# Kernel tuning notes

Measured on AMD Instinct MI355X. Metric: run time of the kernel, lower is better.

## Reference

```python
import jax, jax.numpy as jnp
import numpy as np

L = 5          # num_layer
D = 128        # emb_dim
F = 16         # raw node/edge feature dim
N = 50000      # nodes
E = 800000     # edges
BN_EPS = 1e-5


def _bn(z, g, b):
    # BatchNorm1d forward with batch statistics (training-mode math)
    m = z.mean(axis=0)
    v = z.var(axis=0)
    return (z - m) * jax.lax.rsqrt(v + BN_EPS) * g + b


def setup_inputs() -> dict:
    key = jax.random.key(0)
    ks = jax.random.split(key, 8)
    s = lambda *sh: 0.05  # weight scale
    return {
        "x": jax.random.normal(ks[0], (N, F), jnp.float32),
        "edge_index": jax.random.randint(ks[1], (2, E), 0, N, jnp.int32),
        "edge_attr": jax.random.normal(ks[2], (E, F), jnp.float32),
        "W_node": jax.random.normal(ks[3], (F, D), jnp.float32) * 0.05,
        "b_node": jnp.zeros((D,), jnp.float32),
        "We": jax.random.normal(ks[4], (L, F, D), jnp.float32) * 0.05,
        "be": jnp.zeros((L, D), jnp.float32),
        "eps_gin": jnp.zeros((L,), jnp.float32),
        "W1": jax.random.normal(ks[5], (L, D, 2 * D), jnp.float32) * 0.05,
        "b1": jnp.zeros((L, 2 * D), jnp.float32),
        "g1": jnp.ones((L, 2 * D), jnp.float32),
        "beta1": jnp.zeros((L, 2 * D), jnp.float32),
        "W2": jax.random.normal(ks[6], (L, 2 * D, D), jnp.float32) * 0.05,
        "b2": jnp.zeros((L, D), jnp.float32),
        "g_bn": jnp.ones((L, D), jnp.float32),
        "beta_bn": jnp.zeros((L, D), jnp.float32),
    }


def reference(x, edge_index, edge_attr, W_node, b_node, We, be, eps_gin,
              W1, b1, g1, beta1, W2, b2, g_bn, beta_bn):
    src, dst = edge_index[0], edge_index[1]
    n = x.shape[0]
    h = x @ W_node + b_node                       # node encoder: [N, D]
    for l in range(L):
        e = edge_attr @ We[l] + be[l]             # edge encoder: [E, D]
        msg = jax.nn.relu(h[src] + e)             # gather + message
        agg = jax.ops.segment_sum(msg, dst, num_segments=n)  # scatter-add
        z = (1.0 + eps_gin[l]) * h + agg
        z = _bn(z @ W1[l] + b1[l], g1[l], beta1[l])  # GIN MLP hidden
        z = jax.nn.relu(z)
        z = z @ W2[l] + b2[l]                     # GIN MLP out: [N, D]
        z = _bn(z, g_bn[l], beta_bn[l])           # per-layer BatchNorm
        if l < L - 1:
            z = jax.nn.relu(z)                    # dropout is identity (p=0)
        h = z + h                                 # residual
    return h                                      # JK = 'last'
```

## Files before the change

kernel.cpp:

```cpp
#include <hip/hip_runtime.h>
#include <hip/hip_bf16.h>

#define NN 50000
#define EE 800000
#define DD 128
#define FF 16
#define LL 5
#define NB 782
#define NPART (NB * 4)

typedef __attribute__((ext_vector_type(8))) short bf16x8;
typedef __attribute__((ext_vector_type(4))) float f32x4;

__device__ __forceinline__ unsigned short f2bf(float f) {
    union { float f; unsigned int u; } v; v.f = f;
    unsigned int u = v.u;
    unsigned int r = (u + 0x7fffu + ((u >> 16) & 1u)) >> 16;
    return (unsigned short)r;
}
__device__ __forceinline__ float bf2f(unsigned short s) {
    union { unsigned int u; float f; } v; v.u = ((unsigned int)s) << 16;
    return v.f;
}
#define BFLO(u) __uint_as_float((unsigned int)(u) << 16)
#define BFHI(u) __uint_as_float((unsigned int)(u) & 0xffff0000u)

__global__ void k_node_enc(const float* __restrict__ x, const float* __restrict__ Wn,
                           const float* __restrict__ bn, float* __restrict__ h,
                           unsigned short* __restrict__ h_bf)
{
    const int t = blockIdx.x * 256 + threadIdx.x;
    const int i = t >> 7, d = t & 127;
    const float4* x4 = (const float4*)(x + (size_t)i * 16);
    float4 a0 = x4[0], a1 = x4[1], a2 = x4[2], a3 = x4[3];
    float acc = bn[d];
    acc += a0.x*Wn[0*128+d] + a0.y*Wn[1*128+d] + a0.z*Wn[2*128+d] + a0.w*Wn[3*128+d];
    acc += a1.x*Wn[4*128+d] + a1.y*Wn[5*128+d] + a1.z*Wn[6*128+d] + a1.w*Wn[7*128+d];
    acc += a2.x*Wn[8*128+d] + a2.y*Wn[9*128+d] + a2.z*Wn[10*128+d] + a2.w*Wn[11*128+d];
    acc += a3.x*Wn[12*128+d] + a3.y*Wn[13*128+d] + a3.z*Wn[14*128+d] + a3.w*Wn[15*128+d];
    h[t] = acc;
    h_bf[t] = f2bf(acc);
}

__global__ void k_count(const int* __restrict__ ei, int* __restrict__ counts)
{
    const int e = blockIdx.x * 256 + threadIdx.x;
    atomicAdd(&counts[ei[EE + e]], 1);
}

__global__ __launch_bounds__(1024) void k_scan(int* __restrict__ counts, int* __restrict__ row_ptr)
{
    __shared__ int wsum[16];
    __shared__ int carry;
    const int tid = threadIdx.x, lane = tid & 63, w = tid >> 6;
    if (tid == 0) carry = 0;
    __syncthreads();
    for (int base = 0; base < NN; base += 1024) {
        const int i = base + tid;
        const int v = (i < NN) ? counts[i] : 0;
        int x = v;
        #pragma unroll
        for (int off = 1; off < 64; off <<= 1) {
            const int t = __shfl_up(x, off);
            if (lane >= off) x += t;
        }
        if (lane == 63) wsum[w] = x;
        __syncthreads();
        int woff = 0, total = 0;
        #pragma unroll
        for (int j = 0; j < 16; ++j) { const int s = wsum[j]; total += s; if (j < w) woff += s; }
        const int ex = carry + woff + x - v;
        if (i < NN) { row_ptr[i] = ex; counts[i] = ex; }
        __syncthreads();
        if (tid == 0) carry += total;
        __syncthreads();
    }
    if (tid == 0) row_ptr[NN] = carry;
}

__global__ void k_fill(const int* __restrict__ ei, const float* __restrict__ ea,
                       int* __restrict__ cursor, int* __restrict__ src_perm,
                       unsigned short* __restrict__ ea_bf)
{
    const int e = blockIdx.x * 256 + threadIdx.x;
    const int dst = ei[EE + e];
    const int p = atomicAdd(&cursor[dst], 1);
    src_perm[p] = ei[e];
    const float4* s4 = (const float4*)(ea + (size_t)e * 16);
    const float4 a0 = s4[0], a1 = s4[1], a2 = s4[2], a3 = s4[3];
    union { bf16x8 v; unsigned short u[8]; } o0, o1;
    o0.u[0]=f2bf(a0.x); o0.u[1]=f2bf(a0.y); o0.u[2]=f2bf(a0.z); o0.u[3]=f2bf(a0.w);
    o0.u[4]=f2bf(a1.x); o0.u[5]=f2bf(a1.y); o0.u[6]=f2bf(a1.z); o0.u[7]=f2bf(a1.w);
    o1.u[0]=f2bf(a2.x); o1.u[1]=f2bf(a2.y); o1.u[2]=f2bf(a2.z); o1.u[3]=f2bf(a2.w);
    o1.u[4]=f2bf(a3.x); o1.u[5]=f2bf(a3.y); o1.u[6]=f2bf(a3.z); o1.u[7]=f2bf(a3.w);
    bf16x8* dp = (bf16x8*)(ea_bf + (size_t)p * 16);
    dp[0] = o0.v; dp[1] = o1.v;
}

__global__ void k_pack(const float* __restrict__ W1, const float* __restrict__ W2,
                       unsigned short* __restrict__ Wp1, unsigned short* __restrict__ Wp2)
{
    int t = blockIdx.x * 256 + threadIdx.x;
    const int total = LL * 32768;
    if (t < total) {
        const int l = t >> 15, r = t & 32767;
        const int j = r & 7, lane = (r >> 3) & 63, kt = (r >> 9) & 3, nt = r >> 11;
        const int k = kt * 32 + (lane >> 4) * 8 + j;
        const int n = nt * 16 + (lane & 15);
        Wp1[t] = f2bf(W1[(size_t)l * 32768 + k * 256 + n]);
    } else {
        t -= total;
        const int l = t >> 15, r = t & 32767;
        const int j = r & 7, lane = (r >> 3) & 63, kt = (r >> 9) & 7, nt = r >> 12;
        const int k = kt * 32 + (lane >> 4) * 8 + j;
        const int n = nt * 16 + (lane & 15);
        Wp2[t] = f2bf(W2[(size_t)l * 32768 + k * 128 + n]);
    }
}

__global__ __launch_bounds__(256) void k_agg(
    const unsigned short* __restrict__ h_bf, const unsigned short* __restrict__ ea_bf,
    const float* __restrict__ We_l, const float* __restrict__ be_l,
    const float* __restrict__ eps_gin, const int l,
    const int* __restrict__ row_ptr, const int* __restrict__ src_perm,
    unsigned short* __restrict__ z_bf)
{
    const int wv = threadIdx.x >> 6;
    const int v  = blockIdx.x * 4 + wv;
    const int lane = threadIdx.x & 63;
    const int c2 = lane * 2;
    float2 w[16];
    #pragma unroll
    for (int f = 0; f < 16; ++f) w[f] = *(const float2*)(We_l + f * 128 + c2);
    const float2 bed = *(const float2*)(be_l + c2);
    const float epsv = 1.0f + eps_gin[l];
    const int kbeg = __builtin_amdgcn_readfirstlane(row_ptr[v]);
    const int kend = __builtin_amdgcn_readfirstlane(row_ptr[v + 1]);
    float2 acc0 = {0.f,0.f}, acc1 = {0.f,0.f}, acc2 = {0.f,0.f}, acc3 = {0.f,0.f};

#define EDGE_DOT(EA, EB, HQ, OUT) do {                                      \
        float ex_ = bed.x, ey_ = bed.y, a_;                                 \
        a_ = BFLO(EA.x); ex_ += a_*w[0].x;  ey_ += a_*w[0].y;               \
        a_ = BFHI(EA.x); ex_ += a_*w[1].x;  ey_ += a_*w[1].y;               \
        a_ = BFLO(EA.y); ex_ += a_*w[2].x;  ey_ += a_*w[2].y;               \
        a_ = BFHI(EA.y); ex_ += a_*w[3].x;  ey_ += a_*w[3].y;               \
        a_ = BFLO(EA.z); ex_ += a_*w[4].x;  ey_ += a_*w[4].y;               \
        a_ = BFHI(EA.z); ex_ += a_*w[5].x;  ey_ += a_*w[5].y;               \
        a_ = BFLO(EA.w); ex_ += a_*w[6].x;  ey_ += a_*w[6].y;               \
        a_ = BFHI(EA.w); ex_ += a_*w[7].x;  ey_ += a_*w[7].y;               \
        a_ = BFLO(EB.x); ex_ += a_*w[8].x;  ey_ += a_*w[8].y;               \
        a_ = BFHI(EB.x); ex_ += a_*w[9].x;  ey_ += a_*w[9].y;               \
        a_ = BFLO(EB.y); ex_ += a_*w[10].x; ey_ += a_*w[10].y;              \
        a_ = BFHI(EB.y); ex_ += a_*w[11].x; ey_ += a_*w[11].y;              \
        a_ = BFLO(EB.z); ex_ += a_*w[12].x; ey_ += a_*w[12].y;              \
        a_ = BFHI(EB.z); ex_ += a_*w[13].x; ey_ += a_*w[13].y;              \
        a_ = BFLO(EB.w); ex_ += a_*w[14].x; ey_ += a_*w[14].y;              \
        a_ = BFHI(EB.w); ex_ += a_*w[15].x; ey_ += a_*w[15].y;              \
        const float mx_ = BFLO(HQ) + ex_, my_ = BFHI(HQ) + ey_;             \
        OUT.x += mx_ > 0.f ? mx_ : 0.f;                                     \
        OUT.y += my_ > 0.f ? my_ : 0.f;                                     \
    } while (0)

    uint4 ce0, ce1, ce2, ce3, ce4, ce5, ce6, ce7;
    unsigned int ch0, ch1, ch2, ch3;
    int vs0, vs1, vs2, vs3;

    int k = kbeg;
    if (k < kend) {
        const int a0 = __builtin_amdgcn_readfirstlane(src_perm[k]);
        const int a1 = __builtin_amdgcn_readfirstlane(src_perm[k + 1]);
        const int a2 = __builtin_amdgcn_readfirstlane(src_perm[k + 2]);
        const int a3 = __builtin_amdgcn_readfirstlane(src_perm[k + 3]);
        ch0 = *(const unsigned int*)(h_bf + (size_t)a0 * 128 + c2);
        ch1 = *(const unsigned int*)(h_bf + (size_t)a1 * 128 + c2);
        ch2 = *(const unsigned int*)(h_bf + (size_t)a2 * 128 + c2);
        ch3 = *(const unsigned int*)(h_bf + (size_t)a3 * 128 + c2);
        const uint4* ep = (const uint4*)(ea_bf + (size_t)k * 16);
        ce0 = ep[0]; ce1 = ep[1]; ce2 = ep[2]; ce3 = ep[3];
        ce4 = ep[4]; ce5 = ep[5]; ce6 = ep[6]; ce7 = ep[7];
        vs0 = src_perm[k + 4]; vs1 = src_perm[k + 5];
        vs2 = src_perm[k + 6]; vs3 = src_perm[k + 7];
    }
    for (; k < kend; k += 4) {
        const int fs0 = src_perm[k + 8],  fs1 = src_perm[k + 9];
        const int fs2 = src_perm[k + 10], fs3 = src_perm[k + 11];
        const int b0 = __builtin_amdgcn_readfirstlane(vs0);
        const int b1 = __builtin_amdgcn_readfirstlane(vs1);
        const int b2 = __builtin_amdgcn_readfirstlane(vs2);
        const int b3 = __builtin_amdgcn_readfirstlane(vs3);
        const unsigned int nh0 = *(const unsigned int*)(h_bf + (size_t)b0 * 128 + c2);
        const unsigned int nh1 = *(const unsigned int*)(h_bf + (size_t)b1 * 128 + c2);
        const unsigned int nh2 = *(const unsigned int*)(h_bf + (size_t)b2 * 128 + c2);
        const unsigned int nh3 = *(const unsigned int*)(h_bf + (size_t)b3 * 128 + c2);
        const uint4* np_ = (const uint4*)(ea_bf + (size_t)(k + 4) * 16);
        const uint4 ne0 = np_[0], ne1 = np_[1], ne2 = np_[2], ne3 = np_[3];
        const uint4 ne4 = np_[4], ne5 = np_[5], ne6 = np_[6], ne7 = np_[7];
        __builtin_amdgcn_sched_barrier(0);
        EDGE_DOT(ce0, ce1, ch0, acc0);
        if (k + 1 < kend) EDGE_DOT(ce2, ce3, ch1, acc1);
        if (k + 2 < kend) EDGE_DOT(ce4, ce5, ch2, acc2);
        if (k + 3 < kend) EDGE_DOT(ce6, ce7, ch3, acc3);
        ce0=ne0; ce1=ne1; ce2=ne2; ce3=ne3; ce4=ne4; ce5=ne5; ce6=ne6; ce7=ne7;
        ch0=nh0; ch1=nh1; ch2=nh2; ch3=nh3;
        vs0=fs0; vs1=fs1; vs2=fs2; vs3=fs3;
    }
#undef EDGE_DOT
    const unsigned int hv = *(const unsigned int*)(h_bf + (size_t)v * 128 + c2);
    const float zx = epsv * BFLO(hv) + ((acc0.x + acc1.x) + (acc2.x + acc3.x));
    const float zy = epsv * BFHI(hv) + ((acc0.y + acc1.y) + (acc2.y + acc3.y));
    const unsigned int zp = (unsigned int)f2bf(zx) | ((unsigned int)f2bf(zy) << 16);
    *(unsigned int*)(z_bf + (size_t)v * 128 + c2) = zp;
}

__global__ __launch_bounds__(256) void k_gemmB(
    const unsigned short* __restrict__ z_bf,
    const unsigned short* __restrict__ Wp,
    unsigned short* __restrict__ t_bf,
    float* __restrict__ ps, float* __restrict__ pq)
{
    __shared__ __align__(16) unsigned short zs[64 * 136];
    const int tid = threadIdx.x;
    const int r0 = blockIdx.x * 64;
    {
        const int rb = tid >> 4, c0 = (tid & 15) * 8;
        const bf16x8 zero = {0,0,0,0,0,0,0,0};
        #pragma unroll
        for (int r = 0; r < 4; ++r) {
            const int row = r * 16 + rb, g = r0 + row;
            *(bf16x8*)(&zs[row * 136 + c0]) =
                (g < NN) ? *(const bf16x8*)(z_bf + (size_t)g * 128 + c0) : zero;
        }
    }
    __syncthreads();
    const int w = tid >> 6, l6 = tid & 63, m = l6 & 15, quad = l6 >> 4;
    const f32x4 z4 = {0.f, 0.f, 0.f, 0.f};
    f32x4 acc[16] = {z4,z4,z4,z4,z4,z4,z4,z4,z4,z4,z4,z4,z4,z4,z4,z4};
    const bf16x8* Wv = (const bf16x8*)Wp;
    #pragma unroll
    for (int kt = 0; kt < 4; ++kt) {
        const bf16x8 a = *(const bf16x8*)(&zs[(w * 16 + m) * 136 + kt * 32 + quad * 8]);
        #pragma unroll
        for (int ct = 0; ct < 16; ++ct) {
            const bf16x8 b = Wv[(ct * 4 + kt) * 64 + l6];
            acc[ct] = __builtin_amdgcn_mfma_f32_16x16x32_bf16(a, b, acc[ct], 0, 0, 0);
        }
    }
    const int rowb = r0 + w * 16 + quad * 4;
    #pragma unroll
    for (int ct = 0; ct < 16; ++ct) {
        const int col = ct * 16 + m;
        float ssum = 0.f, ssq = 0.f;
        #pragma unroll
        for (int r = 0; r < 4; ++r) {
            const float val = acc[ct][r];
            if (rowb + r < NN) t_bf[(size_t)(rowb + r) * 256 + col] = f2bf(val);
            ssum += val; ssq += val * val;
        }
        ssum += __shfl_xor(ssum, 16); ssum += __shfl_xor(ssum, 32);
        ssq  += __shfl_xor(ssq , 16); ssq  += __shfl_xor(ssq , 32);
        if (quad == 0) {
            ps[(size_t)col * NPART + blockIdx.x * 4 + w] = ssum;
            pq[(size_t)col * NPART + blockIdx.x * 4 + w] = ssq;
        }
    }
}

__global__ void k_bnstat(const float* __restrict__ ps, const float* __restrict__ pq,
                         const float* __restrict__ g, const float* __restrict__ beta,
                         float* __restrict__ sc, float* __restrict__ sh)
{
    const int c = blockIdx.x;
    const int tid = threadIdx.x;
    const float* pr = ps + (size_t)c * NPART;
    const float* qr = pq + (size_t)c * NPART;
    float s = 0.f, q = 0.f;
    for (int i = tid; i < NPART; i += 256) { s += pr[i]; q += qr[i]; }
    #pragma unroll
    for (int off = 1; off < 64; off <<= 1) { s += __shfl_xor(s, off); q += __shfl_xor(q, off); }
    __shared__ float ls[4], lq[4];
    const int wv = tid >> 6;
    if ((tid & 63) == 0) { ls[wv] = s; lq[wv] = q; }
    __syncthreads();
    if (tid == 0) {
        const float S = ls[0] + ls[1] + ls[2] + ls[3];
        const float Q = lq[0] + lq[1] + lq[2] + lq[3];
        const float mean = S * (1.0f / NN);
        const float var  = Q * (1.0f / NN) - mean * mean;
        const float rs = rsqrtf(var + 1e-5f);
        const float scale = g[c] * rs;
        sc[c] = scale;
        sh[c] = beta[c] - mean * scale;
    }
}

__global__ __launch_bounds__(256) void k_gemmD(
    const unsigned short* __restrict__ t_bf,
    const float* __restrict__ sc1, const float* __restrict__ sh1,
    const unsigned short* __restrict__ Wp,
    unsigned short* __restrict__ vb,
    float* __restrict__ ps, float* __restrict__ pq)
{
    __shared__ __align__(16) unsigned short us[64 * 264];
    const int tid = threadIdx.x;
    const int r0 = blockIdx.x * 64;
    {
        const int rb = tid >> 5, c0 = (tid & 31) * 8;
        const float4 s0 = *(const float4*)(sc1 + c0), s1 = *(const float4*)(sc1 + c0 + 4);
        const float4 b0 = *(const float4*)(sh1 + c0), b1 = *(const float4*)(sh1 + c0 + 4);
        const bf16x8 zero = {0,0,0,0,0,0,0,0};
        #pragma unroll
        for (int rr = 0; rr < 8; ++rr) {
            const int row = rr * 8 + rb, g = r0 + row;
            union { bf16x8 v; unsigned short u[8]; } in, o;
            if (g < NN) {
                in.v = *(const bf16x8*)(t_bf + (size_t)g * 256 + c0);
                float xv;
                xv = bf2f(in.u[0])*s0.x + b0.x; o.u[0] = f2bf(xv > 0.f ? xv : 0.f);
                xv = bf2f(in.u[1])*s0.y + b0.y; o.u[1] = f2bf(xv > 0.f ? xv : 0.f);
                xv = bf2f(in.u[2])*s0.z + b0.z; o.u[2] = f2bf(xv > 0.f ? xv : 0.f);
                xv = bf2f(in.u[3])*s0.w + b0.w; o.u[3] = f2bf(xv > 0.f ? xv : 0.f);
                xv = bf2f(in.u[4])*s1.x + b1.x; o.u[4] = f2bf(xv > 0.f ? xv : 0.f);
                xv = bf2f(in.u[5])*s1.y + b1.y; o.u[5] = f2bf(xv > 0.f ? xv : 0.f);
                xv = bf2f(in.u[6])*s1.z + b1.z; o.u[6] = f2bf(xv > 0.f ? xv : 0.f);
                xv = bf2f(in.u[7])*s1.w + b1.w; o.u[7] = f2bf(xv > 0.f ? xv : 0.f);
            } else {
                o.v = zero;
            }
            *(bf16x8*)(&us[row * 264 + c0]) = o.v;
        }
    }
    __syncthreads();
    const int w = tid >> 6, l6 = tid & 63, m = l6 & 15, quad = l6 >> 4;
    const f32x4 z4 = {0.f, 0.f, 0.f, 0.f};
    f32x4 acc[8] = {z4,z4,z4,z4,z4,z4,z4,z4};
    const bf16x8* Wv = (const bf16x8*)Wp;
    #pragma unroll
    for (int kt = 0; kt < 8; ++kt) {
        const bf16x8 a = *(const bf16x8*)(&us[(w * 16 + m) * 264 + kt * 32 + quad * 8]);
        #pragma unroll
        for (int ct = 0; ct < 8; ++ct) {
            const bf16x8 b = Wv[(ct * 8 + kt) * 64 + l6];
            acc[ct] = __builtin_amdgcn_mfma_f32_16x16x32_bf16(a, b, acc[ct], 0, 0, 0);
        }
    }
    const int rowb = r0 + w * 16 + quad * 4;
    #pragma unroll
    for (int ct = 0; ct < 8; ++ct) {
        const int col = ct * 16 + m;
        float ssum = 0.f, ssq = 0.f;
        #pragma unroll
        for (int r = 0; r < 4; ++r) {
            const float val = acc[ct][r];
            if (rowb + r < NN) vb[(size_t)(rowb + r) * 128 + col] = f2bf(val);
            ssum += val; ssq += val * val;
        }
        ssum += __shfl_xor(ssum, 16); ssum += __shfl_xor(ssum, 32);
        ssq  += __shfl_xor(ssq , 16); ssq  += __shfl_xor(ssq , 32);
        if (quad == 0) {
            ps[(size_t)col * NPART + blockIdx.x * 4 + w] = ssum;
            pq[(size_t)col * NPART + blockIdx.x * 4 + w] = ssq;
        }
    }
}

__global__ void k_fin(const unsigned short* __restrict__ vb,
                      const float* __restrict__ sc2, const float* __restrict__ sh2,
                      float* __restrict__ h, unsigned short* __restrict__ h_bf,
                      const int do_relu)
{
    const int t = blockIdx.x * 256 + threadIdx.x;
    const int base = t * 8;
    const int c = base & 127;
    union { bf16x8 v; unsigned short u[8]; } in, ob;
    in.v = *(const bf16x8*)(vb + base);
    const float4 s0 = *(const float4*)(sc2 + c), s1 = *(const float4*)(sc2 + c + 4);
    const float4 b0 = *(const float4*)(sh2 + c), b1 = *(const float4*)(sh2 + c + 4);
    float4 h0 = *(const float4*)(h + base), h1 = *(const float4*)(h + base + 4);
    float z;
    z = bf2f(in.u[0])*s0.x + b0.x; if (do_relu) z = z > 0.f ? z : 0.f; h0.x += z;
    z = bf2f(in.u[1])*s0.y + b0.y; if (do_relu) z = z > 0.f ? z : 0.f; h0.y += z;
    z = bf2f(in.u[2])*s0.z + b0.z; if (do_relu) z = z > 0.f ? z : 0.f; h0.z += z;
    z = bf2f(in.u[3])*s0.w + b0.w; if (do_relu) z = z > 0.f ? z : 0.f; h0.w += z;
    z = bf2f(in.u[4])*s1.x + b1.x; if (do_relu) z = z > 0.f ? z : 0.f; h1.x += z;
    z = bf2f(in.u[5])*s1.y + b1.y; if (do_relu) z = z > 0.f ? z : 0.f; h1.y += z;
    z = bf2f(in.u[6])*s1.z + b1.z; if (do_relu) z = z > 0.f ? z : 0.f; h1.z += z;
    z = bf2f(in.u[7])*s1.w + b1.w; if (do_relu) z = z > 0.f ? z : 0.f; h1.w += z;
    *(float4*)(h + base) = h0;
    *(float4*)(h + base + 4) = h1;
    ob.u[0]=f2bf(h0.x); ob.u[1]=f2bf(h0.y); ob.u[2]=f2bf(h0.z); ob.u[3]=f2bf(h0.w);
    ob.u[4]=f2bf(h1.x); ob.u[5]=f2bf(h1.y); ob.u[6]=f2bf(h1.z); ob.u[7]=f2bf(h1.w);
    *(bf16x8*)(h_bf + base) = ob.v;
}

extern "C" void kernel_launch(void* const* d_in, const int* in_sizes, int n_in,
                              void* d_out, int out_size, void* d_ws, size_t ws_size,
                              hipStream_t stream)
{
    const float* x       = (const float*)d_in[0];
    const int*   ei      = (const int*)  d_in[1];
    const float* ea      = (const float*)d_in[2];
    const float* W_node  = (const float*)d_in[3];
    const float* b_node  = (const float*)d_in[4];
    const float* We      = (const float*)d_in[5];
    const float* be      = (const float*)d_in[6];
    const float* eps_gin = (const float*)d_in[7];
    const float* W1      = (const float*)d_in[8];
    const float* g1      = (const float*)d_in[10];
    const float* beta1   = (const float*)d_in[11];
    const float* W2      = (const float*)d_in[12];
    const float* g_bn    = (const float*)d_in[14];
    const float* beta_bn = (const float*)d_in[15];

    float* h = (float*)d_out;

    char* W = (char*)d_ws;
    int*   counts   = (int*)  (W + 0);
    int*   row_ptr  = (int*)  (W + 200000);
    float* sc1      = (float*)(W + 400064);
    float* sh1      = (float*)(W + 401088);
    float* sc2      = (float*)(W + 402112);
    float* sh2      = (float*)(W + 402624);
    float* ps1      = (float*)(W + 403136);
    float* pq1      = (float*)(W + 3606208);
    float* ps2      = (float*)(W + 6809280);
    float* pq2      = (float*)(W + 8410816);
    int*   src_perm = (int*)  (W + 10012352);
    unsigned short* ea_bf = (unsigned short*)(W + 13212416);
    unsigned short* Wp1   = (unsigned short*)(W + 38812928);
    unsigned short* Wp2   = (unsigned short*)(W + 39140608);
    unsigned short* z_bf  = (unsigned short*)(W + 39468288);
    unsigned short* t_bf  = (unsigned short*)(W + 52268288);
    unsigned short* h_bf  = (unsigned short*)(W + 77868288);
    unsigned short* vb    = z_bf;

    (void)hipMemsetAsync(counts, 0, 200000, stream);
    (void)hipMemsetAsync(src_perm + EE, 0, 64, stream);

    k_node_enc<<<dim3(NN * DD / 256), dim3(256), 0, stream>>>(x, W_node, b_node, h, h_bf);
    k_count<<<dim3(EE / 256), dim3(256), 0, stream>>>(ei, counts);
    k_scan<<<dim3(1), dim3(1024), 0, stream>>>(counts, row_ptr);
    k_fill<<<dim3(EE / 256), dim3(256), 0, stream>>>(ei, ea, counts, src_perm, ea_bf);
    k_pack<<<dim3(2 * LL * 32768 / 256), dim3(256), 0, stream>>>(W1, W2, Wp1, Wp2);

    for (int l = 0; l < LL; ++l) {
        k_agg<<<dim3(NN / 4), dim3(256), 0, stream>>>(
            h_bf, ea_bf, We + (size_t)l * FF * DD, be + (size_t)l * DD,
            eps_gin, l, row_ptr, src_perm, z_bf);
        k_gemmB<<<dim3(NB), dim3(256), 0, stream>>>(
            z_bf, Wp1 + (size_t)l * 32768, t_bf, ps1, pq1);
        k_bnstat<<<dim3(256), dim3(256), 0, stream>>>(
            ps1, pq1, g1 + (size_t)l * 256, beta1 + (size_t)l * 256, sc1, sh1);
        k_gemmD<<<dim3(NB), dim3(256), 0, stream>>>(
            t_bf, sc1, sh1, Wp2 + (size_t)l * 32768, vb, ps2, pq2);
        k_bnstat<<<dim3(128), dim3(256), 0, stream>>>(
            ps2, pq2, g_bn + (size_t)l * 128, beta_bn + (size_t)l * 128, sc2, sh2);
        k_fin<<<dim3(NN * DD / 8 / 256), dim3(256), 0, stream>>>(
            vb, sc2, sh2, h, h_bf, (l < LL - 1) ? 1 : 0);
    }
}
```

Baseline: 1.051 ms.

## Fuse BN statistics via atomics and hold weight tiles in registers for GEMMs

```diff
diff --git a/kernel.cpp b/kernel.cpp
--- a/kernel.cpp
+++ b/kernel.cpp
@@ -7,7 +7,6 @@
 #define FF 16
 #define LL 5
 #define NB 782
-#define NPART (NB * 4)
 
 typedef __attribute__((ext_vector_type(8))) short bf16x8;
 typedef __attribute__((ext_vector_type(4))) float f32x4;
@@ -216,97 +215,95 @@
     const unsigned short* __restrict__ z_bf,
     const unsigned short* __restrict__ Wp,
     unsigned short* __restrict__ t_bf,
-    float* __restrict__ ps, float* __restrict__ pq)
-{
-    __shared__ __align__(16) unsigned short zs[64 * 136];
+    float* __restrict__ ps1, float* __restrict__ pq1)
+{
     const int tid = threadIdx.x;
+    const int w = tid >> 6, l6 = tid & 63, m = l6 & 15, quad = l6 >> 4;
     const int r0 = blockIdx.x * 64;
+    const bf16x8* Wv = (const bf16x8*)Wp;
+    bf16x8 b[4][4];
+    #pragma unroll
+    for (int ct = 0; ct < 4; ++ct)
+        #pragma unroll
+        for (int kt = 0; kt < 4; ++kt)
+            b[ct][kt] = Wv[((w * 4 + ct) * 4 + kt) * 64 + l6];
+
+    const bf16x8 zero8 = {0,0,0,0,0,0,0,0};
+    const f32x4 z4 = {0.f, 0.f, 0.f, 0.f};
+    float rs_[4] = {0.f,0.f,0.f,0.f}, rq_[4] = {0.f,0.f,0.f,0.f};
+
+    bf16x8 a[4], an[4];
     {
-        const int rb = tid >> 4, c0 = (tid & 15) * 8;
-        const bf16x8 zero = {0,0,0,0,0,0,0,0};
-        #pragma unroll
-        for (int r = 0; r < 4; ++r) {
-            const int row = r * 16 + rb, g = r0 + row;
-            *(bf16x8*)(&zs[row * 136 + c0]) =
-                (g < NN) ? *(const bf16x8*)(z_bf + (size_t)g * 128 + c0) : zero;
-        }
-    }
-    __syncthreads();
-    const int w = tid >> 6, l6 = tid & 63, m = l6 & 15, quad = l6 >> 4;
-    const f32x4 z4 = {0.f, 0.f, 0.f, 0.f};
-    f32x4 acc[16] = {z4,z4,z4,z4,z4,z4,z4,z4,z4,z4,z4,z4,z4,z4,z4,z4};
-    const bf16x8* Wv = (const bf16x8*)Wp;
-    #pragma unroll
-    for (int kt = 0; kt < 4; ++kt) {
-        const bf16x8 a = *(const bf16x8*)(&zs[(w * 16 + m) * 136 + kt * 32 + quad * 8]);
-        #pragma unroll
-        for (int ct = 0; ct < 16; ++ct) {
-            const bf16x8 b = Wv[(ct * 4 + kt) * 64 + l6];
-            acc[ct] = __builtin_amdgcn_mfma_f32_16x16x32_bf16(a, b, acc[ct], 0, 0, 0);
-        }
-    }
-    const int rowb = r0 + w * 16 + quad * 4;
-    #pragma unroll
-    for (int ct = 0; ct < 16; ++ct) {
-        const int col = ct * 16 + m;
-        float ssum = 0.f, ssq = 0.f;
-        #pragma unroll
-        for (int r = 0; r < 4; ++r) {
-            const float val = acc[ct][r];
-            if (rowb + r < NN) t_bf[(size_t)(rowb + r) * 256 + col] = f2bf(val);
-            ssum += val; ssq += val * val;
-        }
-        ssum += __shfl_xor(ssum, 16); ssum += __shfl_xor(ssum, 32);
-        ssq  += __shfl_xor(ssq , 16); ssq  += __shfl_xor(ssq , 32);
+        const int row = r0 + m;
+        #pragma unroll
+        for (int kt = 0; kt < 4; ++kt)
+            a[kt] = (row < NN) ? *(const bf16x8*)(z_bf + (size_t)row * 128 + kt * 32 + quad * 8) : zero8;
+    }
+    #pragma unroll
+    for (int rt = 0; rt < 4; ++rt) {
+        if (rt < 3) {
+            const int row = r0 + (rt + 1) * 16 + m;
+            #pragma unroll
+            for (int kt = 0; kt < 4; ++kt)
+                an[kt] = (row < NN) ? *(const bf16x8*)(z_bf + (size_t)row * 128 + kt * 32 + quad * 8) : zero8;
+        }
+        f32x4 acc[4] = {z4, z4, z4, z4};
+        #pragma unroll
+        for (int kt = 0; kt < 4; ++kt)
+            #pragma unroll
+            for (int ct = 0; ct < 4; ++ct)
+                acc[ct] = __builtin_amdgcn_mfma_f32_16x16x32_bf16(a[kt], b[ct][kt], acc[ct], 0, 0, 0);
+        const int rowb = r0 + rt * 16 + quad * 4;
+        #pragma unroll
+        for (int ct = 0; ct < 4; ++ct) {
+            const int col = w * 64 + ct * 16 + m;
+            #pragma unroll
+            for (int r = 0; r < 4; ++r) {
+                const float val = acc[ct][r];
+                if (rowb + r < NN) t_bf[(size_t)(rowb + r) * 256 + col] = f2bf(val);
+                rs_[ct] += val; rq_[ct] += val * val;
+            }
+        }
+        #pragma unroll
+        for (int kt = 0; kt < 4; ++kt) a[kt] = an[kt];
+    }
+    #pragma unroll
+    for (int ct = 0; ct < 4; ++ct) {
+        float ss = rs_[ct], sq = rq_[ct];
+        ss += __shfl_xor(ss, 16); ss += __shfl_xor(ss, 32);
+        sq += __shfl_xor(sq, 16); sq += __shfl_xor(sq, 32);
         if (quad == 0) {
-            ps[(size_t)col * NPART + blockIdx.x * 4 + w] = ssum;
-            pq[(size_t)col * NPART + blockIdx.x * 4 + w] = ssq;
-        }
-    }
-}
-
-__global__ void k_bnstat(const float* __restrict__ ps, const float* __restrict__ pq,
-                         const float* __restrict__ g, const float* __restrict__ beta,
-                         float* __restrict__ sc, float* __restrict__ sh)
-{
-    const int c = blockIdx.x;
-    const int tid = threadIdx.x;
-    const float* pr = ps + (size_t)c * NPART;
-    const float* qr = pq + (size_t)c * NPART;
-    float s = 0.f, q = 0.f;
-    for (int i = tid; i < NPART; i += 256) { s += pr[i]; q += qr[i]; }
-    #pragma unroll
-    for (int off = 1; off < 64; off <<= 1) { s += __shfl_xor(s, off); q += __shfl_xor(q, off); }
-    __shared__ float ls[4], lq[4];
-    const int wv = tid >> 6;
-    if ((tid & 63) == 0) { ls[wv] = s; lq[wv] = q; }
-    __syncthreads();
-    if (tid == 0) {
-        const float S = ls[0] + ls[1] + ls[2] + ls[3];
-        const float Q = lq[0] + lq[1] + lq[2] + lq[3];
-        const float mean = S * (1.0f / NN);
-        const float var  = Q * (1.0f / NN) - mean * mean;
-        const float rs = rsqrtf(var + 1e-5f);
-        const float scale = g[c] * rs;
-        sc[c] = scale;
-        sh[c] = beta[c] - mean * scale;
+            const int col = w * 64 + ct * 16 + m;
+            atomicAdd(&ps1[col], ss);
+            atomicAdd(&pq1[col], sq);
+        }
     }
 }
 
 __global__ __launch_bounds__(256) void k_gemmD(
     const unsigned short* __restrict__ t_bf,
-    const float* __restrict__ sc1, const float* __restrict__ sh1,
+    const float* __restrict__ ps1, const float* __restrict__ pq1,
+    const float* __restrict__ g1, const float* __restrict__ be1,
     const unsigned short* __restrict__ Wp,
     unsigned short* __restrict__ vb,
-    float* __restrict__ ps, float* __restrict__ pq)
+    float* __restrict__ ps2, float* __restrict__ pq2)
 {
     __shared__ __align__(16) unsigned short us[64 * 264];
+    __shared__ __align__(16) float scf[256], shf[256];
     const int tid = threadIdx.x;
+    {
+        const float mean = ps1[tid] * (1.0f / NN);
+        const float var  = pq1[tid] * (1.0f / NN) - mean * mean;
+        const float sc = g1[tid] * rsqrtf(var + 1e-5f);
+        scf[tid] = sc;
+        shf[tid] = be1[tid] - mean * sc;
+    }
+    __syncthreads();
     const int r0 = blockIdx.x * 64;
     {
         const int rb = tid >> 5, c0 = (tid & 31) * 8;
-        const float4 s0 = *(const float4*)(sc1 + c0), s1 = *(const float4*)(sc1 + c0 + 4);
-        const float4 b0 = *(const float4*)(sh1 + c0), b1 = *(const float4*)(sh1 + c0 + 4);
+        const float4 s0 = *(const float4*)(scf + c0), s1 = *(const float4*)(scf + c0 + 4);
+        const float4 b0 = *(const float4*)(shf + c0), b1 = *(const float4*)(shf + c0 + 4);
         const bf16x8 zero = {0,0,0,0,0,0,0,0};
         #pragma unroll
         for (int rr = 0; rr < 8; ++rr) {
@@ -331,50 +328,76 @@
     }
     __syncthreads();
     const int w = tid >> 6, l6 = tid & 63, m = l6 & 15, quad = l6 >> 4;
+    const bf16x8* Wv = (const bf16x8*)Wp;
+    bf16x8 b[2][8];
+    #pragma unroll
+    for (int ct = 0; ct < 2; ++ct)
+        #pragma unroll
+        for (int kt = 0; kt < 8; ++kt)
+            b[ct][kt] = Wv[((w * 2 + ct) * 8 + kt) * 64 + l6];
+
     const f32x4 z4 = {0.f, 0.f, 0.f, 0.f};
-    f32x4 acc[8] = {z4,z4,z4,z4,z4,z4,z4,z4};
-    const bf16x8* Wv = (const bf16x8*)Wp;
-    #pragma unroll
-    for (int kt = 0; kt < 8; ++kt) {
-        const bf16x8 a = *(const bf16x8*)(&us[(w * 16 + m) * 264 + kt * 32 + quad * 8]);
-        #pragma unroll
-        for (int ct = 0; ct < 8; ++ct) {
-            const bf16x8 b = Wv[(ct * 8 + kt) * 64 + l6];
-            acc[ct] = __builtin_amdgcn_mfma_f32_16x16x32_bf16(a, b, acc[ct], 0, 0, 0);
-        }
-    }
-    const int rowb = r0 + w * 16 + quad * 4;
-    #pragma unroll
-    for (int ct = 0; ct < 8; ++ct) {
-        const int col = ct * 16 + m;
-        float ssum = 0.f, ssq = 0.f;
-        #pragma unroll
-        for (int r = 0; r < 4; ++r) {
-            const float val = acc[ct][r];
-            if (rowb + r < NN) vb[(size_t)(rowb + r) * 128 + col] = f2bf(val);
-            ssum += val; ssq += val * val;
-        }
-        ssum += __shfl_xor(ssum, 16); ssum += __shfl_xor(ssum, 32);
-        ssq  += __shfl_xor(ssq , 16); ssq  += __shfl_xor(ssq , 32);
+    float rs_[2] = {0.f,0.f}, rq_[2] = {0.f,0.f};
+    #pragma unroll
+    for (int rt = 0; rt < 4; ++rt) {
+        bf16x8 a[8];
+        #pragma unroll
+        for (int kt = 0; kt < 8; ++kt)
+            a[kt] = *(const bf16x8*)(&us[(rt * 16 + m) * 264 + kt * 32 + quad * 8]);
+        f32x4 acc[2] = {z4, z4};
+        #pragma unroll
+        for (int kt = 0; kt < 8; ++kt)
+            #pragma unroll
+            for (int ct = 0; ct < 2; ++ct)
+                acc[ct] = __builtin_amdgcn_mfma_f32_16x16x32_bf16(a[kt], b[ct][kt], acc[ct], 0, 0, 0);
+        const int rowb = r0 + rt * 16 + quad * 4;
+        #pragma unroll
+        for (int ct = 0; ct < 2; ++ct) {
+            const int col = w * 32 + ct * 16 + m;
+            #pragma unroll
+            for (int r = 0; r < 4; ++r) {
+                const float val = acc[ct][r];
+                if (rowb + r < NN) vb[(size_t)(rowb + r) * 128 + col] = f2bf(val);
+                rs_[ct] += val; rq_[ct] += val * val;
+            }
+        }
+    }
+    #pragma unroll
+    for (int ct = 0; ct < 2; ++ct) {
+        float ss = rs_[ct], sq = rq_[ct];
+        ss += __shfl_xor(ss, 16); ss += __shfl_xor(ss, 32);
+        sq += __shfl_xor(sq, 16); sq += __shfl_xor(sq, 32);
         if (quad == 0) {
-            ps[(size_t)col * NPART + blockIdx.x * 4 + w] = ssum;
-            pq[(size_t)col * NPART + blockIdx.x * 4 + w] = ssq;
+            const int col = w * 32 + ct * 16 + m;
+            atomicAdd(&ps2[col], ss);
+            atomicAdd(&pq2[col], sq);
         }
     }
 }
 
 __global__ void k_fin(const unsigned short* __restrict__ vb,
-                      const float* __restrict__ sc2, const float* __restrict__ sh2,
+                      const float* __restrict__ ps2, const float* __restrict__ pq2,
+                      const float* __restrict__ g2, const float* __restrict__ be2,
                       float* __restrict__ h, unsigned short* __restrict__ h_bf,
                       const int do_relu)
 {
-    const int t = blockIdx.x * 256 + threadIdx.x;
+    __shared__ __align__(16) float scf[128], shf[128];
+    const int tid = threadIdx.x;
+    if (tid < 128) {
+        const float mean = ps2[tid] * (1.0f / NN);
+        const float var  = pq2[tid] * (1.0f / NN) - mean * mean;
+        const float sc = g2[tid] * rsqrtf(var + 1e-5f);
+        scf[tid] = sc;
+        shf[tid] = be2[tid] - mean * sc;
+    }
+    __syncthreads();
+    const int t = blockIdx.x * 256 + tid;
     const int base = t * 8;
     const int c = base & 127;
     union { bf16x8 v; unsigned short u[8]; } in, ob;
     in.v = *(const bf16x8*)(vb + base);
-    const float4 s0 = *(const float4*)(sc2 + c), s1 = *(const float4*)(sc2 + c + 4);
-    const float4 b0 = *(const float4*)(sh2 + c), b1 = *(const float4*)(sh2 + c + 4);
+    const float4 s0 = *(const float4*)(scf + c), s1 = *(const float4*)(scf + c + 4);
+    const float4 b0 = *(const float4*)(shf + c), b1 = *(const float4*)(shf + c + 4);
     float4 h0 = *(const float4*)(h + base), h1 = *(const float4*)(h + base + 4);
     float z;
     z = bf2f(in.u[0])*s0.x + b0.x; if (do_relu) z = z > 0.f ? z : 0.f; h0.x += z;
@@ -416,21 +439,15 @@
     char* W = (char*)d_ws;
     int*   counts   = (int*)  (W + 0);
     int*   row_ptr  = (int*)  (W + 200000);
-    float* sc1      = (float*)(W + 400064);
-    float* sh1      = (float*)(W + 401088);
-    float* sc2      = (float*)(W + 402112);
-    float* sh2      = (float*)(W + 402624);
-    float* ps1      = (float*)(W + 403136);
-    float* pq1      = (float*)(W + 3606208);
-    float* ps2      = (float*)(W + 6809280);
-    float* pq2      = (float*)(W + 8410816);
-    int*   src_perm = (int*)  (W + 10012352);
-    unsigned short* ea_bf = (unsigned short*)(W + 13212416);
-    unsigned short* Wp1   = (unsigned short*)(W + 38812928);
-    unsigned short* Wp2   = (unsigned short*)(W + 39140608);
-    unsigned short* z_bf  = (unsigned short*)(W + 39468288);
-    unsigned short* t_bf  = (unsigned short*)(W + 52268288);
-    unsigned short* h_bf  = (unsigned short*)(W + 77868288);
+    float* stats    = (float*)(W + 400064);
+    float* ps1 = stats, *pq1 = stats + 256, *ps2 = stats + 512, *pq2 = stats + 640;
+    int*   src_perm = (int*)  (W + 403136);
+    unsigned short* ea_bf = (unsigned short*)(W + 3603200);
+    unsigned short* Wp1   = (unsigned short*)(W + 29203712);
+    unsigned short* Wp2   = (unsigned short*)(W + 29531392);
+    unsigned short* z_bf  = (unsigned short*)(W + 29859072);
+    unsigned short* t_bf  = (unsigned short*)(W + 42659072);
+    unsigned short* h_bf  = (unsigned short*)(W + 68259072);
     unsigned short* vb    = z_bf;
 
     (void)hipMemsetAsync(counts, 0, 200000, stream);
@@ -443,18 +460,17 @@
     k_pack<<<dim3(2 * LL * 32768 / 256), dim3(256), 0, stream>>>(W1, W2, Wp1, Wp2);
 
     for (int l = 0; l < LL; ++l) {
+        (void)hipMemsetAsync(stats, 0, 3072, stream);
         k_agg<<<dim3(NN / 4), dim3(256), 0, stream>>>(
             h_bf, ea_bf, We + (size_t)l * FF * DD, be + (size_t)l * DD,
             eps_gin, l, row_ptr, src_perm, z_bf);
         k_gemmB<<<dim3(NB), dim3(256), 0, stream>>>(
             z_bf, Wp1 + (size_t)l * 32768, t_bf, ps1, pq1);
-        k_bnstat<<<dim3(256), dim3(256), 0, stream>>>(
-            ps1, pq1, g1 + (size_t)l * 256, beta1 + (size_t)l * 256, sc1, sh1);
         k_gemmD<<<dim3(NB), dim3(256), 0, stream>>>(
-            t_bf, sc1, sh1, Wp2 + (size_t)l * 32768, vb, ps2, pq2);
-        k_bnstat<<<dim3(128), dim3(256), 0, stream>>>(
-            ps2, pq2, g_bn + (size_t)l * 128, beta_bn + (size_t)l * 128, sc2, sh2);
+            t_bf, ps1, pq1, g1 + (size_t)l * 256, beta1 + (size_t)l * 256,
+            Wp2 + (size_t)l * 32768, vb, ps2, pq2);
         k_fin<<<dim3(NN * DD / 8 / 256), dim3(256), 0, stream>>>(
-            vb, sc2, sh2, h, h_bf, (l < LL - 1) ? 1 : 0);
-    }
-}
+            vb, ps2, pq2, g_bn + (size_t)l * 128, beta_bn + (size_t)l * 128,
+            h, h_bf, (l < LL - 1) ? 1 : 0);
+    }
+}
```

New measurement: 927.3 us. 11.8% less time.
